# Performance work log

Hardware: AMD Instinct MI355X
Metric: run time of the kernel (lower is better)

## Reference

```python
import jax, jax.numpy as jnp
import numpy as np


def setup_inputs() -> dict:
    key = jax.random.key(0)
    kq, kk, kv = jax.random.split(key, 3)
    n, m, d, v = 4096, 4096, 1024, 1024
    Q = jax.random.normal(kq, (n, d), dtype=jnp.float32)
    K = jax.random.normal(kk, (m, d), dtype=jnp.float32)
    V = jax.random.normal(kv, (m, v), dtype=jnp.float32)
    return {"Q": Q, "K": K, "V": V}


def reference(Q, K, V):
    d = K.shape[-1]
    scale = d ** (-0.5)
    logits = jnp.matmul(Q, K.T)                      # [n, m]
    # Faithful to source: softmax over dim=1 (keys), THEN scaled by d**-0.5
    scores = jax.nn.softmax(logits, axis=1) * scale  # [n, m]
    return jnp.matmul(scores, V)                     # [n, v]
```

## Files before the change

### kernel.cpp

```cpp
#include <hip/hip_runtime.h>
#include <hip/hip_bf16.h>

typedef _Float16 f16x8 __attribute__((ext_vector_type(8)));
typedef _Float16 f16x4 __attribute__((ext_vector_type(4)));
typedef float f32x4 __attribute__((ext_vector_type(4)));

__device__ __forceinline__ void async_ld16(_Float16* lds, const _Float16* g) {
    __builtin_amdgcn_global_load_lds(
        (const __attribute__((address_space(1))) void*)g,
        (__attribute__((address_space(3))) void*)lds, 16, 0, 0);
}

struct CDesc {
    float *p0, *p1, *p2, *p3;
    int l0, l1, l2, l3;
};

__global__ __launch_bounds__(256) void gemm_bt(
    const _Float16* __restrict__ A,
    const _Float16* __restrict__ B,
    int M, int N, int Ks, int lda, int ldb, CDesc cd)
{
    __shared__ _Float16 At[2][128 * 32];
    __shared__ _Float16 Bt[2][128 * 32];

    const int tid  = threadIdx.x;
    const int wave = tid >> 6;
    const int lane = tid & 63;

    const int gx = gridDim.x, gy = gridDim.y;
    int bx = blockIdx.x, by = blockIdx.y;
    if ((gy & 7) == 0) {
        const int bid = bx + gx * by;
        const int x = bid & 7;
        const int j = bid >> 3;
        bx = j % gx;
        by = x + 8 * (j / gx);
    }
    const int row0 = by * 128;
    const int col0 = bx * 128;

    const int wr = (wave >> 1) * 64;
    const int wc = (wave & 1) * 64;
    const int quad = lane >> 4;
    const int l16  = lane & 15;

    f32x4 acc[4][4] = {};

    const int srow  = lane >> 2;
    const int skoff = (lane & 3) * 8;
    const size_t K64a = (size_t)64 * lda;
    const size_t K64b = (size_t)64 * ldb;

    const int z = blockIdx.z;
    const _Float16* Ab = A + (size_t)row0 * lda + (size_t)z * Ks;
    const _Float16* Bb = B + (size_t)col0 * ldb + (size_t)z * Ks;

    const _Float16* pa = Ab + (size_t)(wave * 16 + srow) * lda + skoff;
    const _Float16* pb = Bb + (size_t)(wave * 16 + srow) * ldb + skoff;

    async_ld16(At[0] + wave * 512,       pa);
    async_ld16(At[0] + (wave + 4) * 512, pa + K64a);
    async_ld16(Bt[0] + wave * 512,       pb);
    async_ld16(Bt[0] + (wave + 4) * 512, pb + K64b);
    __syncthreads();

    int cur = 0;
    for (int k0 = 0; k0 < Ks; k0 += 32) {
        const int nxt = cur ^ 1;
        if (k0 + 32 < Ks) {
            const _Float16* qa = pa + k0 + 32;
            const _Float16* qb = pb + k0 + 32;
            async_ld16(At[nxt] + wave * 512,       qa);
            async_ld16(At[nxt] + (wave + 4) * 512, qa + K64a);
            async_ld16(Bt[nxt] + wave * 512,       qb);
            async_ld16(Bt[nxt] + (wave + 4) * 512, qb + K64b);
        }

        f16x8 af[4], bf[4];
        #pragma unroll
        for (int r = 0; r < 4; ++r)
            af[r] = *(const f16x8*)&At[cur][(wr + r * 16 + l16) * 32 + quad * 8];
        #pragma unroll
        for (int c = 0; c < 4; ++c)
            bf[c] = *(const f16x8*)&Bt[cur][(wc + c * 16 + l16) * 32 + quad * 8];

        #pragma unroll
        for (int r = 0; r < 4; ++r)
            #pragma unroll
            for (int c = 0; c < 4; ++c)
                acc[r][c] = __builtin_amdgcn_mfma_f32_16x16x32_f16(af[r], bf[c], acc[r][c], 0, 0, 0);

        __syncthreads();
        cur = nxt;
    }

    float* Cb; int ldc;
    if      (z == 0) { Cb = cd.p0; ldc = cd.l0; }
    else if (z == 1) { Cb = cd.p1; ldc = cd.l1; }
    else if (z == 2) { Cb = cd.p2; ldc = cd.l2; }
    else             { Cb = cd.p3; ldc = cd.l3; }

    #pragma unroll
    for (int r = 0; r < 4; ++r) {
        const int growb = row0 + wr + r * 16 + quad * 4;
        #pragma unroll
        for (int c = 0; c < 4; ++c) {
            const int gcol = col0 + wc + c * 16 + l16;
            #pragma unroll
            for (int i = 0; i < 4; ++i)
                __builtin_nontemporal_store(
                    acc[r][c][i], &Cb[(size_t)(growb + i) * ldc + gcol]);
        }
    }
}

__global__ __launch_bounds__(256) void softmax_rows(
    float* __restrict__ S, float scale)
{
    __shared__ float red[4];
    const int row = blockIdx.x;
    const int tid = threadIdx.x;
    const int wave = tid >> 6;
    const float4* Sr = (const float4*)(S + (size_t)row * 4096);

    float4 x[4];
    #pragma unroll
    for (int i = 0; i < 4; ++i) x[i] = Sr[tid + i * 256];

    float mx = -3.402823466e+38f;
    #pragma unroll
    for (int i = 0; i < 4; ++i)
        mx = fmaxf(mx, fmaxf(fmaxf(x[i].x, x[i].y), fmaxf(x[i].z, x[i].w)));
    #pragma unroll
    for (int off = 32; off > 0; off >>= 1) mx = fmaxf(mx, __shfl_down(mx, off));
    if ((tid & 63) == 0) red[wave] = mx;
    __syncthreads();
    mx = fmaxf(fmaxf(red[0], red[1]), fmaxf(red[2], red[3]));
    __syncthreads();

    float sum = 0.0f;
    #pragma unroll
    for (int i = 0; i < 4; ++i) {
        x[i].x = __expf(x[i].x - mx);
        x[i].y = __expf(x[i].y - mx);
        x[i].z = __expf(x[i].z - mx);
        x[i].w = __expf(x[i].w - mx);
        sum += x[i].x + x[i].y + x[i].z + x[i].w;
    }
    #pragma unroll
    for (int off = 32; off > 0; off >>= 1) sum += __shfl_down(sum, off);
    if ((tid & 63) == 0) red[wave] = sum;
    __syncthreads();
    sum = red[0] + red[1] + red[2] + red[3];

    const float inv = scale / sum;
    f16x4* Pr = (f16x4*)((_Float16*)S + (size_t)row * 8192);
    #pragma unroll
    for (int i = 0; i < 4; ++i) {
        f16x4 h;
        h.x = (_Float16)(x[i].x * inv);
        h.y = (_Float16)(x[i].y * inv);
        h.z = (_Float16)(x[i].z * inv);
        h.w = (_Float16)(x[i].w * inv);
        Pr[tid + i * 256] = h;
    }
}

__global__ __launch_bounds__(256) void cvt2_f32_f16(
    const float4* __restrict__ a, f16x4* __restrict__ da, int n4a,
    const float4* __restrict__ b, f16x4* __restrict__ db, int n4b)
{
    int i = blockIdx.x * 256 + threadIdx.x;
    const int stride = gridDim.x * 256;
    const int tot = n4a + n4b;
    for (; i < tot; i += stride) {
        const float4* s = (i < n4a) ? (a + i) : (b + (i - n4a));
        f16x4* d = (i < n4a) ? (da + i) : (db + (i - n4a));
        float4 v = *s;
        f16x4 h;
        h.x = (_Float16)v.x; h.y = (_Float16)v.y;
        h.z = (_Float16)v.z; h.w = (_Float16)v.w;
        *d = h;
    }
}

__global__ __launch_bounds__(256) void transpose_cvt(
    const float* __restrict__ V, _Float16* __restrict__ Vt, int rows, int cols)
{
    __shared__ float tile[32][33];
    const int c0 = blockIdx.x * 32;
    const int r0 = blockIdx.y * 32;
    const int tx = threadIdx.x & 31;
    const int ty = threadIdx.x >> 5;
    #pragma unroll
    for (int i = 0; i < 4; ++i)
        tile[ty * 4 + i][tx] = V[(size_t)(r0 + ty * 4 + i) * cols + c0 + tx];
    __syncthreads();
    #pragma unroll
    for (int i = 0; i < 4; ++i)
        Vt[(size_t)(c0 + ty * 4 + i) * rows + r0 + tx] = (_Float16)tile[tx][ty * 4 + i];
}

__global__ __launch_bounds__(256) void reduce_add(
    float4* __restrict__ out,
    const float* __restrict__ p1, int ld1,
    const float* __restrict__ p2, int ld2,
    const float* __restrict__ p3, int ld3,
    int nparts, int rows)
{
    int i = blockIdx.x * 256 + threadIdx.x;
    const int stride = gridDim.x * 256;
    const int tot = rows * 256;
    for (; i < tot; i += stride) {
        const int r = i >> 8, c = i & 255;
        float4 v = out[i];
        float4 a = ((const float4*)(p1 + (size_t)r * ld1))[c];
        v.x += a.x; v.y += a.y; v.z += a.z; v.w += a.w;
        if (nparts > 1) {
            float4 b = ((const float4*)(p2 + (size_t)r * ld2))[c];
            v.x += b.x; v.y += b.y; v.z += b.z; v.w += b.w;
        }
        if (nparts > 2) {
            float4 d = ((const float4*)(p3 + (size_t)r * ld3))[c];
            v.x += d.x; v.y += d.y; v.z += d.z; v.w += d.w;
        }
        out[i] = v;
    }
}

extern "C" void kernel_launch(void* const* d_in, const int* in_sizes, int n_in,
                              void* d_out, int out_size, void* d_ws, size_t ws_size,
                              hipStream_t stream) {
    const float* Q = (const float*)d_in[0];
    const float* K = (const float*)d_in[1];
    const float* V = (const float*)d_in[2];
    float* out = (float*)d_out;

    const int n = 4096, m = 4096, d = 1024, vdim = 1024;
    const float scale = 0.03125f;

    char* w = (char*)d_ws;
    _Float16* Qh = (_Float16*)w;
    _Float16* Kh = (_Float16*)(w + (8u << 20));
    _Float16* Vt = (_Float16*)(w + (16u << 20));
    char* rest = w + (24u << 20);
    size_t avail = ws_size > (24u << 20) ? ws_size - (24u << 20) : 0;

    int nc, sk;
    if      (avail >= (size_t)4096 * 16384)                        { nc = 4096; sk = 2; }
    else if (avail >= (size_t)2048 * 16384 + (size_t)2048 * 4096)  { nc = 2048; sk = 4; }
    else if (avail >= (size_t)1024 * 16384 + (size_t)1024 * 4096)  { nc = 1024; sk = 4; }
    else                                                           { nc = 512;  sk = 4; }

    float* S = (float*)rest;
    float* pd1 = S + 2048;
    float* pd2 = S + 3072;
    float* pde = S + (size_t)nc * 4096;

    cvt2_f32_f16<<<dim3(2048), dim3(256), 0, stream>>>(
        (const float4*)Q, (f16x4*)Qh, n * d / 4,
        (const float4*)K, (f16x4*)Kh, m * d / 4);
    transpose_cvt<<<dim3(vdim / 32, m / 32), dim3(256), 0, stream>>>(V, Vt, m, vdim);

    for (int r0 = 0; r0 < n; r0 += nc) {
        CDesc cs; cs.p0 = S; cs.l0 = m;
        cs.p1 = cs.p2 = cs.p3 = S; cs.l1 = cs.l2 = cs.l3 = m;
        gemm_bt<<<dim3(m / 128, nc / 128, 1), dim3(256), 0, stream>>>(
            Qh + (size_t)r0 * d, Kh, nc, m, d, d, d, cs);

        softmax_rows<<<dim3(nc), dim3(256), 0, stream>>>(S, scale);

        float* o0 = out + (size_t)r0 * vdim;
        CDesc co;
        co.p0 = o0;  co.l0 = vdim;
        co.p1 = pd1; co.l1 = 4096;
        co.p2 = pd2; co.l2 = 4096;
        co.p3 = pde; co.l3 = vdim;
        gemm_bt<<<dim3(vdim / 128, nc / 128, sk), dim3(256), 0, stream>>>(
            (const _Float16*)S, Vt, nc, vdim, m / sk, 2 * m, m, co);

        reduce_add<<<dim3(1024), dim3(256), 0, stream>>>(
            (float4*)o0, pd1, 4096, pd2, 4096, pde, vdim, sk - 1, nc);
    }
}
```

Measured before the change: 215.6 us.

## Replace split-K partial buffers and reduce kernel with atomic accumulation

The second GEMM's split-K partials are now atomically added straight into a zeroed output, which removes the partial-sum buffers and the separate reduce_add kernel. The Q/K conversion, the V transpose-convert and the output zeroing are merged into one prep launch. This cuts launch count and the extra write and read of partial results, at the cost of float atomics on the output and nondeterministic summation order.

```diff
diff --git a/kernel.cpp b/kernel.cpp
--- a/kernel.cpp
+++ b/kernel.cpp
@@ -11,15 +11,11 @@
         (__attribute__((address_space(3))) void*)lds, 16, 0, 0);
 }
 
-struct CDesc {
-    float *p0, *p1, *p2, *p3;
-    int l0, l1, l2, l3;
-};
-
 __global__ __launch_bounds__(256) void gemm_bt(
     const _Float16* __restrict__ A,
     const _Float16* __restrict__ B,
-    int M, int N, int Ks, int lda, int ldb, CDesc cd)
+    float* __restrict__ C,
+    int M, int N, int Ks, int lda, int ldb, int ldc, int accum)
 {
     __shared__ _Float16 At[2][128 * 32];
     __shared__ _Float16 Bt[2][128 * 32];
@@ -95,22 +91,22 @@
         cur = nxt;
     }
 
-    float* Cb; int ldc;
-    if      (z == 0) { Cb = cd.p0; ldc = cd.l0; }
-    else if (z == 1) { Cb = cd.p1; ldc = cd.l1; }
-    else if (z == 2) { Cb = cd.p2; ldc = cd.l2; }
-    else             { Cb = cd.p3; ldc = cd.l3; }
-
     #pragma unroll
     for (int r = 0; r < 4; ++r) {
         const int growb = row0 + wr + r * 16 + quad * 4;
         #pragma unroll
         for (int c = 0; c < 4; ++c) {
             const int gcol = col0 + wc + c * 16 + l16;
-            #pragma unroll
-            for (int i = 0; i < 4; ++i)
-                __builtin_nontemporal_store(
-                    acc[r][c][i], &Cb[(size_t)(growb + i) * ldc + gcol]);
+            if (accum) {
+                #pragma unroll
+                for (int i = 0; i < 4; ++i)
+                    atomicAdd(&C[(size_t)(growb + i) * ldc + gcol], acc[r][c][i]);
+            } else {
+                #pragma unroll
+                for (int i = 0; i < 4; ++i)
+                    __builtin_nontemporal_store(
+                        acc[r][c][i], &C[(size_t)(growb + i) * ldc + gcol]);
+            }
         }
     }
 }
@@ -167,65 +163,46 @@
     }
 }
 
-__global__ __launch_bounds__(256) void cvt2_f32_f16(
-    const float4* __restrict__ a, f16x4* __restrict__ da, int n4a,
-    const float4* __restrict__ b, f16x4* __restrict__ db, int n4b)
+__global__ __launch_bounds__(256) void prep(
+    const float* __restrict__ Q, _Float16* __restrict__ Qh, int nQ4,
+    const float* __restrict__ Kf, _Float16* __restrict__ Kh, int nK4,
+    const float* __restrict__ V, _Float16* __restrict__ Vt, int rows, int cols,
+    float4* __restrict__ outz, int nz4)
 {
-    int i = blockIdx.x * 256 + threadIdx.x;
-    const int stride = gridDim.x * 256;
-    const int tot = n4a + n4b;
-    for (; i < tot; i += stride) {
-        const float4* s = (i < n4a) ? (a + i) : (b + (i - n4a));
-        f16x4* d = (i < n4a) ? (da + i) : (db + (i - n4a));
-        float4 v = *s;
-        f16x4 h;
-        h.x = (_Float16)v.x; h.y = (_Float16)v.y;
-        h.z = (_Float16)v.z; h.w = (_Float16)v.w;
-        *d = h;
-    }
-}
-
-__global__ __launch_bounds__(256) void transpose_cvt(
-    const float* __restrict__ V, _Float16* __restrict__ Vt, int rows, int cols)
-{
-    __shared__ float tile[32][33];
-    const int c0 = blockIdx.x * 32;
-    const int r0 = blockIdx.y * 32;
-    const int tx = threadIdx.x & 31;
-    const int ty = threadIdx.x >> 5;
-    #pragma unroll
-    for (int i = 0; i < 4; ++i)
-        tile[ty * 4 + i][tx] = V[(size_t)(r0 + ty * 4 + i) * cols + c0 + tx];
-    __syncthreads();
-    #pragma unroll
-    for (int i = 0; i < 4; ++i)
-        Vt[(size_t)(c0 + ty * 4 + i) * rows + r0 + tx] = (_Float16)tile[tx][ty * 4 + i];
-}
-
-__global__ __launch_bounds__(256) void reduce_add(
-    float4* __restrict__ out,
-    const float* __restrict__ p1, int ld1,
-    const float* __restrict__ p2, int ld2,
-    const float* __restrict__ p3, int ld3,
-    int nparts, int rows)
-{
-    int i = blockIdx.x * 256 + threadIdx.x;
-    const int stride = gridDim.x * 256;
-    const int tot = rows * 256;
-    for (; i < tot; i += stride) {
-        const int r = i >> 8, c = i & 255;
-        float4 v = out[i];
-        float4 a = ((const float4*)(p1 + (size_t)r * ld1))[c];
-        v.x += a.x; v.y += a.y; v.z += a.z; v.w += a.w;
-        if (nparts > 1) {
-            float4 b = ((const float4*)(p2 + (size_t)r * ld2))[c];
-            v.x += b.x; v.y += b.y; v.z += b.z; v.w += b.w;
+    const int bid = blockIdx.x;
+    if (bid < 4096) {
+        __shared__ float tile[32][33];
+        const int c0 = (bid & 31) * 32;
+        const int r0 = (bid >> 5) * 32;
+        const int tx = threadIdx.x & 31;
+        const int ty = threadIdx.x >> 5;
+        #pragma unroll
+        for (int i = 0; i < 4; ++i)
+            tile[ty * 4 + i][tx] = V[(size_t)(r0 + ty * 4 + i) * cols + c0 + tx];
+        __syncthreads();
+        #pragma unroll
+        for (int i = 0; i < 4; ++i)
+            Vt[(size_t)(c0 + ty * 4 + i) * rows + r0 + tx] = (_Float16)tile[tx][ty * 4 + i];
+    } else if (bid < 6144) {
+        int i = (bid - 4096) * 256 + threadIdx.x;
+        const int stride = 2048 * 256;
+        const int tot = nQ4 + nK4;
+        const float4* a = (const float4*)Q;
+        const float4* b = (const float4*)Kf;
+        for (; i < tot; i += stride) {
+            const float4* s = (i < nQ4) ? (a + i) : (b + (i - nQ4));
+            f16x4* dd = (i < nQ4) ? ((f16x4*)Qh + i) : ((f16x4*)Kh + (i - nQ4));
+            float4 v = *s;
+            f16x4 h;
+            h.x = (_Float16)v.x; h.y = (_Float16)v.y;
+            h.z = (_Float16)v.z; h.w = (_Float16)v.w;
+            *dd = h;
         }
-        if (nparts > 2) {
-            float4 d = ((const float4*)(p3 + (size_t)r * ld3))[c];
-            v.x += d.x; v.y += d.y; v.z += d.z; v.w += d.w;
-        }
-        out[i] = v;
+    } else {
+        int i = (bid - 6144) * 256 + threadIdx.x;
+        const int stride = 2048 * 256;
+        const float4 zero = {0.f, 0.f, 0.f, 0.f};
+        for (; i < nz4; i += stride) outz[i] = zero;
     }
 }
 
@@ -248,39 +225,25 @@
     size_t avail = ws_size > (24u << 20) ? ws_size - (24u << 20) : 0;
 
     int nc, sk;
-    if      (avail >= (size_t)4096 * 16384)                        { nc = 4096; sk = 2; }
-    else if (avail >= (size_t)2048 * 16384 + (size_t)2048 * 4096)  { nc = 2048; sk = 4; }
-    else if (avail >= (size_t)1024 * 16384 + (size_t)1024 * 4096)  { nc = 1024; sk = 4; }
-    else                                                           { nc = 512;  sk = 4; }
+    if      (avail >= (size_t)4096 * 16384) { nc = 4096; sk = 2; }
+    else if (avail >= (size_t)2048 * 16384) { nc = 2048; sk = 4; }
+    else if (avail >= (size_t)1024 * 16384) { nc = 1024; sk = 4; }
+    else                                    { nc = 512;  sk = 4; }
 
     float* S = (float*)rest;
-    float* pd1 = S + 2048;
-    float* pd2 = S + 3072;
-    float* pde = S + (size_t)nc * 4096;
-
-    cvt2_f32_f16<<<dim3(2048), dim3(256), 0, stream>>>(
-        (const float4*)Q, (f16x4*)Qh, n * d / 4,
-        (const float4*)K, (f16x4*)Kh, m * d / 4);
-    transpose_cvt<<<dim3(vdim / 32, m / 32), dim3(256), 0, stream>>>(V, Vt, m, vdim);
+
+    prep<<<dim3(8192), dim3(256), 0, stream>>>(
+        Q, Qh, n * d / 4, K, Kh, m * d / 4, V, Vt, m, vdim,
+        (float4*)out, n * vdim / 4);
 
     for (int r0 = 0; r0 < n; r0 += nc) {
-        CDesc cs; cs.p0 = S; cs.l0 = m;
-        cs.p1 = cs.p2 = cs.p3 = S; cs.l1 = cs.l2 = cs.l3 = m;
         gemm_bt<<<dim3(m / 128, nc / 128, 1), dim3(256), 0, stream>>>(
-            Qh + (size_t)r0 * d, Kh, nc, m, d, d, d, cs);
+            Qh + (size_t)r0 * d, Kh, S, nc, m, d, d, d, m, 0);
 
         softmax_rows<<<dim3(nc), dim3(256), 0, stream>>>(S, scale);
 
-        float* o0 = out + (size_t)r0 * vdim;
-        CDesc co;
-        co.p0 = o0;  co.l0 = vdim;
-        co.p1 = pd1; co.l1 = 4096;
-        co.p2 = pd2; co.l2 = 4096;
-        co.p3 = pde; co.l3 = vdim;
         gemm_bt<<<dim3(vdim / 128, nc / 128, sk), dim3(256), 0, stream>>>(
-            (const _Float16*)S, Vt, nc, vdim, m / sk, 2 * m, m, co);
-
-        reduce_add<<<dim3(1024), dim3(256), 0, stream>>>(
-            (float4*)o0, pd1, 4096, pd2, 4096, pde, vdim, sk - 1, nc);
-    }
-}
+            (const _Float16*)S, Vt, out + (size_t)r0 * vdim,
+            nc, vdim, m / sk, 2 * m, m, vdim, 1);
+    }
+}
```

Measured after the change: 230.7 us. 1.07x slower.

## Use 256x128 tiles with 512-thread GEMM blocks, fuse prep kernels, fix split-K at 4

Applied to the files above, without the earlier changes.

The GEMM kernel now computes 256x128 output tiles with 8 waves per block instead of 128x128 with 4 waves. This raises reuse of each B tile and halves the number of blocks. The two input-conversion kernels are merged into one launch. The PV GEMM now always splits K four ways, with the extra partial buffer placed in reused workspace when the full chunk fits. Larger tiles mean fewer blocks, which could leave compute units underused, and 512-thread blocks put more pressure on LDS and registers.

```diff
diff --git a/kernel.cpp b/kernel.cpp
--- a/kernel.cpp
+++ b/kernel.cpp
@@ -16,28 +16,28 @@
     int l0, l1, l2, l3;
 };
 
-__global__ __launch_bounds__(256) void gemm_bt(
+__global__ __launch_bounds__(512) void gemm256(
     const _Float16* __restrict__ A,
     const _Float16* __restrict__ B,
-    int M, int N, int Ks, int lda, int ldb, CDesc cd)
-{
-    __shared__ _Float16 At[2][128 * 32];
+    int Ks, int lda, int ldb, CDesc cd)
+{
+    __shared__ _Float16 At[2][256 * 32];
     __shared__ _Float16 Bt[2][128 * 32];
 
     const int tid  = threadIdx.x;
     const int wave = tid >> 6;
     const int lane = tid & 63;
 
-    const int gx = gridDim.x, gy = gridDim.y;
+    const int gx = gridDim.x;
     int bx = blockIdx.x, by = blockIdx.y;
-    if ((gy & 7) == 0) {
+    if ((gridDim.y & 7) == 0) {
         const int bid = bx + gx * by;
         const int x = bid & 7;
         const int j = bid >> 3;
         bx = j % gx;
         by = x + 8 * (j / gx);
     }
-    const int row0 = by * 128;
+    const int row0 = by * 256;
     const int col0 = bx * 128;
 
     const int wr = (wave >> 1) * 64;
@@ -49,32 +49,26 @@
 
     const int srow  = lane >> 2;
     const int skoff = (lane & 3) * 8;
-    const size_t K64a = (size_t)64 * lda;
-    const size_t K64b = (size_t)64 * ldb;
+    const size_t A128 = (size_t)128 * lda;
 
     const int z = blockIdx.z;
-    const _Float16* Ab = A + (size_t)row0 * lda + (size_t)z * Ks;
-    const _Float16* Bb = B + (size_t)col0 * ldb + (size_t)z * Ks;
-
-    const _Float16* pa = Ab + (size_t)(wave * 16 + srow) * lda + skoff;
-    const _Float16* pb = Bb + (size_t)(wave * 16 + srow) * ldb + skoff;
+    const _Float16* pa = A + (size_t)row0 * lda + (size_t)z * Ks
+                           + (size_t)(wave * 16 + srow) * lda + skoff;
+    const _Float16* pb = B + (size_t)col0 * ldb + (size_t)z * Ks
+                           + (size_t)(wave * 16 + srow) * ldb + skoff;
 
     async_ld16(At[0] + wave * 512,       pa);
-    async_ld16(At[0] + (wave + 4) * 512, pa + K64a);
+    async_ld16(At[0] + (wave + 8) * 512, pa + A128);
     async_ld16(Bt[0] + wave * 512,       pb);
-    async_ld16(Bt[0] + (wave + 4) * 512, pb + K64b);
     __syncthreads();
 
     int cur = 0;
     for (int k0 = 0; k0 < Ks; k0 += 32) {
         const int nxt = cur ^ 1;
         if (k0 + 32 < Ks) {
-            const _Float16* qa = pa + k0 + 32;
-            const _Float16* qb = pb + k0 + 32;
-            async_ld16(At[nxt] + wave * 512,       qa);
-            async_ld16(At[nxt] + (wave + 4) * 512, qa + K64a);
-            async_ld16(Bt[nxt] + wave * 512,       qb);
-            async_ld16(Bt[nxt] + (wave + 4) * 512, qb + K64b);
+            async_ld16(At[nxt] + wave * 512,       pa + k0 + 32);
+            async_ld16(At[nxt] + (wave + 8) * 512, pa + k0 + 32 + A128);
+            async_ld16(Bt[nxt] + wave * 512,       pb + k0 + 32);
         }
 
         f16x8 af[4], bf[4];
@@ -167,39 +161,41 @@
     }
 }
 
-__global__ __launch_bounds__(256) void cvt2_f32_f16(
-    const float4* __restrict__ a, f16x4* __restrict__ da, int n4a,
-    const float4* __restrict__ b, f16x4* __restrict__ db, int n4b)
-{
-    int i = blockIdx.x * 256 + threadIdx.x;
-    const int stride = gridDim.x * 256;
-    const int tot = n4a + n4b;
-    for (; i < tot; i += stride) {
-        const float4* s = (i < n4a) ? (a + i) : (b + (i - n4a));
-        f16x4* d = (i < n4a) ? (da + i) : (db + (i - n4a));
-        float4 v = *s;
-        f16x4 h;
-        h.x = (_Float16)v.x; h.y = (_Float16)v.y;
-        h.z = (_Float16)v.z; h.w = (_Float16)v.w;
-        *d = h;
-    }
-}
-
-__global__ __launch_bounds__(256) void transpose_cvt(
+__global__ __launch_bounds__(256) void prep(
+    const float* __restrict__ Q, _Float16* __restrict__ Qh, int nQ4,
+    const float* __restrict__ Kf, _Float16* __restrict__ Kh, int nK4,
     const float* __restrict__ V, _Float16* __restrict__ Vt, int rows, int cols)
 {
-    __shared__ float tile[32][33];
-    const int c0 = blockIdx.x * 32;
-    const int r0 = blockIdx.y * 32;
-    const int tx = threadIdx.x & 31;
-    const int ty = threadIdx.x >> 5;
-    #pragma unroll
-    for (int i = 0; i < 4; ++i)
-        tile[ty * 4 + i][tx] = V[(size_t)(r0 + ty * 4 + i) * cols + c0 + tx];
-    __syncthreads();
-    #pragma unroll
-    for (int i = 0; i < 4; ++i)
-        Vt[(size_t)(c0 + ty * 4 + i) * rows + r0 + tx] = (_Float16)tile[tx][ty * 4 + i];
+    const int bid = blockIdx.x;
+    if (bid < 4096) {
+        __shared__ float tile[32][33];
+        const int c0 = (bid & 31) * 32;
+        const int r0 = (bid >> 5) * 32;
+        const int tx = threadIdx.x & 31;
+        const int ty = threadIdx.x >> 5;
+        #pragma unroll
+        for (int i = 0; i < 4; ++i)
+            tile[ty * 4 + i][tx] = V[(size_t)(r0 + ty * 4 + i) * cols + c0 + tx];
+        __syncthreads();
+        #pragma unroll
+        for (int i = 0; i < 4; ++i)
+            Vt[(size_t)(c0 + ty * 4 + i) * rows + r0 + tx] = (_Float16)tile[tx][ty * 4 + i];
+    } else {
+        int i = (bid - 4096) * 256 + threadIdx.x;
+        const int stride = 2048 * 256;
+        const int tot = nQ4 + nK4;
+        const float4* a = (const float4*)Q;
+        const float4* b = (const float4*)Kf;
+        for (; i < tot; i += stride) {
+            const float4* s = (i < nQ4) ? (a + i) : (b + (i - nQ4));
+            f16x4* dd = (i < nQ4) ? ((f16x4*)Qh + i) : ((f16x4*)Kh + (i - nQ4));
+            float4 v = *s;
+            f16x4 h;
+            h.x = (_Float16)v.x; h.y = (_Float16)v.y;
+            h.z = (_Float16)v.z; h.w = (_Float16)v.w;
+            *dd = h;
+        }
+    }
 }
 
 __global__ __launch_bounds__(256) void reduce_add(
@@ -247,27 +243,25 @@
     char* rest = w + (24u << 20);
     size_t avail = ws_size > (24u << 20) ? ws_size - (24u << 20) : 0;
 
-    int nc, sk;
-    if      (avail >= (size_t)4096 * 16384)                        { nc = 4096; sk = 2; }
-    else if (avail >= (size_t)2048 * 16384 + (size_t)2048 * 4096)  { nc = 2048; sk = 4; }
-    else if (avail >= (size_t)1024 * 16384 + (size_t)1024 * 4096)  { nc = 1024; sk = 4; }
-    else                                                           { nc = 512;  sk = 4; }
+    int nc;
+    if      (avail >= (size_t)4096 * 16384)                       nc = 4096;
+    else if (avail >= (size_t)2048 * 16384 + (size_t)2048 * 4096) nc = 2048;
+    else if (avail >= (size_t)1024 * 16384 + (size_t)1024 * 4096) nc = 1024;
+    else                                                          nc = 512;
 
     float* S = (float*)rest;
     float* pd1 = S + 2048;
     float* pd2 = S + 3072;
-    float* pde = S + (size_t)nc * 4096;
-
-    cvt2_f32_f16<<<dim3(2048), dim3(256), 0, stream>>>(
-        (const float4*)Q, (f16x4*)Qh, n * d / 4,
-        (const float4*)K, (f16x4*)Kh, m * d / 4);
-    transpose_cvt<<<dim3(vdim / 32, m / 32), dim3(256), 0, stream>>>(V, Vt, m, vdim);
+    float* pde = (nc == 4096) ? (float*)w : (S + (size_t)nc * 4096);
+
+    prep<<<dim3(6144), dim3(256), 0, stream>>>(
+        Q, Qh, n * d / 4, K, Kh, m * d / 4, V, Vt, m, vdim);
 
     for (int r0 = 0; r0 < n; r0 += nc) {
-        CDesc cs; cs.p0 = S; cs.l0 = m;
-        cs.p1 = cs.p2 = cs.p3 = S; cs.l1 = cs.l2 = cs.l3 = m;
-        gemm_bt<<<dim3(m / 128, nc / 128, 1), dim3(256), 0, stream>>>(
-            Qh + (size_t)r0 * d, Kh, nc, m, d, d, d, cs);
+        CDesc cs; cs.p0 = cs.p1 = cs.p2 = cs.p3 = S;
+        cs.l0 = cs.l1 = cs.l2 = cs.l3 = m;
+        gemm256<<<dim3(m / 128, nc / 256, 1), dim3(512), 0, stream>>>(
+            Qh + (size_t)r0 * d, Kh, d, d, d, cs);
 
         softmax_rows<<<dim3(nc), dim3(256), 0, stream>>>(S, scale);
 
@@ -277,10 +271,10 @@
         co.p1 = pd1; co.l1 = 4096;
         co.p2 = pd2; co.l2 = 4096;
         co.p3 = pde; co.l3 = vdim;
-        gemm_bt<<<dim3(vdim / 128, nc / 128, sk), dim3(256), 0, stream>>>(
-            (const _Float16*)S, Vt, nc, vdim, m / sk, 2 * m, m, co);
+        gemm256<<<dim3(vdim / 128, nc / 256, 4), dim3(512), 0, stream>>>(
+            (const _Float16*)S, Vt, m / 4, 2 * m, m, co);
 
         reduce_add<<<dim3(1024), dim3(256), 0, stream>>>(
-            (float4*)o0, pd1, 4096, pd2, 4096, pde, vdim, sk - 1, nc);
-    }
-}
+            (float4*)o0, pd1, 4096, pd2, 4096, pde, vdim, 3, nc);
+    }
+}
```

Result: slower. 224.7 us (+4.2%).
